# Performance work log

Measured on AMD Instinct MI355X. Metric: run time of the kernel, lower is better.

Reference implementation:

```python
import jax, jax.numpy as jnp
import numpy as np

DIM = 768
HEADS = 12
HEAD_DIM = DIM // HEADS


def setup_inputs() -> dict:
    key = jax.random.key(0)
    ks = jax.random.split(key, 5)
    B, N = 2, 2048
    x = jax.random.normal(ks[0], (B, N, DIM), dtype=jnp.float32)
    s = 1.0 / np.sqrt(DIM)
    qkv_w = jax.random.normal(ks[1], (3 * DIM, DIM), dtype=jnp.float32) * s
    qkv_b = jnp.zeros((3 * DIM,), dtype=jnp.float32)
    proj_w = jax.random.normal(ks[2], (DIM, DIM), dtype=jnp.float32) * s
    proj_b = jnp.zeros((DIM,), dtype=jnp.float32)
    return {"x": x, "qkv_w": qkv_w, "qkv_b": qkv_b, "proj_w": proj_w, "proj_b": proj_b}


def reference(x, qkv_w, qkv_b, proj_w, proj_b):
    B, N, C = x.shape
    scale = HEAD_DIM ** -0.5
    qkv = x @ qkv_w.T + qkv_b                      # [B,N,3C]
    qkv = qkv.reshape(B, N, 3, HEADS, HEAD_DIM)
    q = qkv[:, :, 0].transpose(0, 2, 1, 3)         # [B,H,N,D]
    k = qkv[:, :, 1].transpose(0, 2, 1, 3)
    v = qkv[:, :, 2].transpose(0, 2, 1, 3)
    attn = jnp.einsum('bhnd,bhmd->bhnm', q, k) * scale
    attn = jax.nn.softmax(attn, axis=-1)
    out = jnp.einsum('bhnm,bhmd->bhnd', attn, v)   # [B,H,N,D]
    out = out.transpose(0, 2, 1, 3).reshape(B, N, C)
    return out @ proj_w.T + proj_b
```

## Files before the change

kernel.cpp:

```cpp
#include <hip/hip_runtime.h>
#include <hip/hip_bf16.h>

typedef __bf16 bf16x8 __attribute__((ext_vector_type(8)));
typedef float f32x4 __attribute__((ext_vector_type(4)));
typedef float f32x16 __attribute__((ext_vector_type(16)));

#define SEQ   2048
#define NHEAD 12
#define NBH   24
#define QSCALE 0.18033688011112042f

#define CP16(g, l) __builtin_amdgcn_global_load_lds( \
    (const __attribute__((address_space(1))) unsigned int*)(g), \
    (__attribute__((address_space(3))) unsigned int*)(l), 16, 0, 0)

__device__ __forceinline__ unsigned short f2bf(float f) {
  unsigned int u = __builtin_bit_cast(unsigned int, f);
  u += 0x7FFFu + ((u >> 16) & 1u);
  return (unsigned short)(u >> 16);
}
__device__ __forceinline__ unsigned int packbf2_trunc(float lo, float hi) {
  return __builtin_amdgcn_perm(__builtin_bit_cast(unsigned int, hi),
                               __builtin_bit_cast(unsigned int, lo), 0x07060302u);
}

#define NX4  786432
#define NW14 442368
__global__ __launch_bounds__(256) void cvt3_kernel(const float4* __restrict__ x,
                                                   const float4* __restrict__ w1,
                                                   const float4* __restrict__ w2,
                                                   ushort4* __restrict__ xo,
                                                   ushort4* __restrict__ w1o,
                                                   ushort4* __restrict__ w2o) {
  int i = blockIdx.x * 256 + threadIdx.x;
  const float4* s;
  ushort4* d;
  int j = i;
  if (i < NX4)               { s = x;  d = xo; }
  else if (i < NX4 + NW14)   { s = w1; d = w1o; j = i - NX4; }
  else                       { s = w2; d = w2o; j = i - (NX4 + NW14); }
  float4 v = s[j];
  ushort4 r;
  r.x = f2bf(v.x); r.y = f2bf(v.y); r.z = f2bf(v.z); r.w = f2bf(v.w);
  d[j] = r;
}

template <int BM, int BN, int MODE>
__global__ __launch_bounds__(256) void gemm_kernel(const unsigned short* __restrict__ X,
                                                   const unsigned short* __restrict__ W,
                                                   const float* __restrict__ bias,
                                                   unsigned short* __restrict__ Qb,
                                                   unsigned short* __restrict__ Kb,
                                                   unsigned short* __restrict__ Vtb,
                                                   float* __restrict__ Out) {
  constexpr int K = 768, BK = 64, NKT = K / BK;
  constexpr int WM = BM / 2, WN = BN / 2;
  constexpr int MT = WM / 16, NT = WN / 16;
  __shared__ __align__(16) unsigned short Xs[2][BM * BK];
  __shared__ __align__(16) unsigned short Ws[2][BN * BK];

  const int tid = threadIdx.x;
  const int w = tid >> 6, lane = tid & 63, quad = lane >> 4, m16 = lane & 15;
  const int wm = w & 1, wn = w >> 1;
  const int row0 = blockIdx.y * BM, col0 = blockIdx.x * BN;

  f32x4 acc[MT][NT];
#pragma unroll
  for (int mt = 0; mt < MT; ++mt)
#pragma unroll
    for (int nt = 0; nt < NT; ++nt) acc[mt][nt] = (f32x4){0.f, 0.f, 0.f, 0.f};

#pragma unroll
  for (int j = 0; j < BM / 32; ++j) {
    int e = tid + 256 * j, r = e >> 3, c8 = e & 7;
    CP16(X + (size_t)(row0 + r) * 768 + ((c8 ^ (r & 7)) << 3), &Xs[0][e * 8]);
  }
#pragma unroll
  for (int j = 0; j < BN / 32; ++j) {
    int e = tid + 256 * j, r = e >> 3, c8 = e & 7;
    CP16(W + (size_t)(col0 + r) * 768 + ((c8 ^ (r & 7)) << 3), &Ws[0][e * 8]);
  }

#pragma unroll 2
  for (int kt = 0; kt < NKT; ++kt) {
    const int cur = kt & 1;
    __syncthreads();

    bf16x8 a[2][MT], b[2][NT];
#pragma unroll
    for (int ks = 0; ks < 2; ++ks) {
      const int sw = ((quad + 4 * ks) ^ (m16 & 7)) << 3;
#pragma unroll
      for (int mt = 0; mt < MT; ++mt)
        a[ks][mt] = *(const bf16x8*)(&Xs[cur][(wm * WM + mt * 16 + m16) * BK + sw]);
#pragma unroll
      for (int nt = 0; nt < NT; ++nt)
        b[ks][nt] = *(const bf16x8*)(&Ws[cur][(wn * WN + nt * 16 + m16) * BK + sw]);
    }

    if (kt < NKT - 1) {
      const int k0n = (kt + 1) * BK, nb = 1 - cur;
#pragma unroll
      for (int j = 0; j < BM / 32; ++j) {
        int e = tid + 256 * j, r = e >> 3, c8 = e & 7;
        CP16(X + (size_t)(row0 + r) * 768 + k0n + ((c8 ^ (r & 7)) << 3), &Xs[nb][e * 8]);
      }
#pragma unroll
      for (int j = 0; j < BN / 32; ++j) {
        int e = tid + 256 * j, r = e >> 3, c8 = e & 7;
        CP16(W + (size_t)(col0 + r) * 768 + k0n + ((c8 ^ (r & 7)) << 3), &Ws[nb][e * 8]);
      }
    }

#pragma unroll
    for (int ks = 0; ks < 2; ++ks)
#pragma unroll
      for (int mt = 0; mt < MT; ++mt)
#pragma unroll
        for (int nt = 0; nt < NT; ++nt)
          acc[mt][nt] = __builtin_amdgcn_mfma_f32_16x16x32_bf16(a[ks][mt], b[ks][nt], acc[mt][nt], 0, 0, 0);
  }

#pragma unroll
  for (int mt = 0; mt < MT; ++mt) {
#pragma unroll
    for (int nt = 0; nt < NT; ++nt) {
      const int m0 = row0 + wm * WM + mt * 16 + quad * 4;
      const int c = col0 + wn * WN + nt * 16 + m16;
      const float bia = bias[c];
      f32x4 v = acc[mt][nt];
      if constexpr (MODE == 0) {
        const int bidx = m0 >> 11, ns = m0 & 2047;
        if (c < 1536) {
          unsigned short* dst;
          float sc;
          int cc;
          if (c < 768) { cc = c; dst = Qb; sc = QSCALE; }
          else         { cc = c - 768; dst = Kb; sc = 1.0f; }
          const int h = cc >> 6, d = cc & 63;
          unsigned short* p = dst + ((size_t)(bidx * NHEAD + h) * SEQ + ns) * 64 + d;
          p[0]   = f2bf((v[0] + bia) * sc);
          p[64]  = f2bf((v[1] + bia) * sc);
          p[128] = f2bf((v[2] + bia) * sc);
          p[192] = f2bf((v[3] + bia) * sc);
        } else {
          const int cc = c - 1536, h = cc >> 6, d = cc & 63;
          const int ns2 = (ns & ~12) | ((ns & 4) << 1) | ((ns & 8) >> 1);
          ushort4 pk;
          pk.x = f2bf(v[0] + bia); pk.y = f2bf(v[1] + bia);
          pk.z = f2bf(v[2] + bia); pk.w = f2bf(v[3] + bia);
          *(ushort4*)(Vtb + ((size_t)(bidx * NHEAD + h) * 64 + d) * SEQ + ns2) = pk;
        }
      } else {
        float* o = Out + (size_t)m0 * 768 + c;
        o[0]       = v[0] + bia;
        o[768]     = v[1] + bia;
        o[2 * 768] = v[2] + bia;
        o[3 * 768] = v[3] + bia;
      }
    }
  }
}

__global__ __launch_bounds__(128) void attn_kernel(const unsigned short* __restrict__ Qb,
                                                   const unsigned short* __restrict__ Kb,
                                                   const unsigned short* __restrict__ Vtb,
                                                   unsigned short* __restrict__ Ab) {
  __shared__ __align__(16) unsigned short Ks[2][64 * 64];
  __shared__ __align__(16) unsigned short Vts[2][64 * 64];

  const int tid = threadIdx.x;
  const int w = tid >> 6, lane = tid & 63, hi = lane >> 5, l32 = lane & 31;
  const int bh = blockIdx.x % NBH, qt = blockIdx.x / NBH;
  const int bb = bh / NHEAD, h = bh % NHEAD;
  const int q0 = qt * 64 + w * 32;

  const unsigned short* Qp = Qb + (size_t)bh * SEQ * 64;
  const unsigned short* Kp = Kb + (size_t)bh * SEQ * 64;
  const unsigned short* Vp = Vtb + (size_t)bh * 64 * SEQ;

  bf16x8 qf[4];
#pragma unroll
  for (int dc = 0; dc < 4; ++dc)
    qf[dc] = *(const bf16x8*)(Qp + (size_t)(q0 + l32) * 64 + dc * 16 + hi * 8);

#pragma unroll
  for (int j = 0; j < 4; ++j) {
    int e = tid + 128 * j, r = e >> 3, c8 = e & 7;
    CP16(Kp + (size_t)r * 64 + ((c8 ^ (r & 7)) << 3), &Ks[0][e * 8]);
    CP16(Vp + (size_t)r * SEQ + ((c8 ^ (r & 7)) << 3), &Vts[0][e * 8]);
  }

  f32x16 o[2] = {};
  float m_i = -3.0e38f, l_i = 0.f;

  for (int kt = 0; kt < 32; ++kt) {
    const int cur = kt & 1;
    __syncthreads();

    const unsigned short* Kc = Ks[cur];
    const unsigned short* Vc = Vts[cur];
    bf16x8 kf[2][4], vf[2][4];
#pragma unroll
    for (int t32 = 0; t32 < 2; ++t32)
#pragma unroll
      for (int dc = 0; dc < 4; ++dc)
        kf[t32][dc] = *(const bf16x8*)(Kc + (t32 * 32 + l32) * 64 + ((((dc << 1) | hi) ^ (l32 & 7)) << 3));
#pragma unroll
    for (int dt = 0; dt < 2; ++dt)
#pragma unroll
      for (int cc = 0; cc < 4; ++cc)
        vf[dt][cc] = *(const bf16x8*)(Vc + (dt * 32 + l32) * 64 + ((((cc << 1) | hi) ^ (l32 & 7)) << 3));

    if (kt < 31) {
      const int kn = kt + 1, nb = 1 - cur;
#pragma unroll
      for (int j = 0; j < 4; ++j) {
        int e = tid + 128 * j, r = e >> 3, c8 = e & 7;
        CP16(Kp + (size_t)(kn * 64 + r) * 64 + ((c8 ^ (r & 7)) << 3), &Ks[nb][e * 8]);
        CP16(Vp + (size_t)r * SEQ + kn * 64 + ((c8 ^ (r & 7)) << 3), &Vts[nb][e * 8]);
      }
    }

    f32x16 st[2];
#pragma unroll
    for (int t32 = 0; t32 < 2; ++t32) {
      f32x16 s = {};
#pragma unroll
      for (int dc = 0; dc < 4; ++dc)
        s = __builtin_amdgcn_mfma_f32_32x32x16_bf16(kf[t32][dc], qf[dc], s, 0, 0, 0);
      st[t32] = s;
    }

    float tmax = st[0][0];
#pragma unroll
    for (int t32 = 0; t32 < 2; ++t32)
#pragma unroll
      for (int e = 0; e < 16; ++e) tmax = fmaxf(tmax, st[t32][e]);
    tmax = fmaxf(tmax, __shfl_xor(tmax, 32));
    const float mnew = fmaxf(m_i, tmax);
    const float alpha = __builtin_amdgcn_exp2f(m_i - mnew);
    float ssum = 0.f;
    unsigned int pf[2][8];
#pragma unroll
    for (int t32 = 0; t32 < 2; ++t32) {
      float pv[16];
#pragma unroll
      for (int e = 0; e < 16; ++e) { pv[e] = __builtin_amdgcn_exp2f(st[t32][e] - mnew); ssum += pv[e]; }
#pragma unroll
      for (int e2 = 0; e2 < 8; ++e2)
        pf[t32][e2] = packbf2_trunc(pv[2 * e2], pv[2 * e2 + 1]);
    }
    ssum += __shfl_xor(ssum, 32);
    l_i = l_i * alpha + ssum;
    m_i = mnew;
    o[0] *= alpha;
    o[1] *= alpha;

#pragma unroll
    for (int t32 = 0; t32 < 2; ++t32) {
#pragma unroll
      for (int hh = 0; hh < 2; ++hh) {
        bf16x8 pfrag = __builtin_bit_cast(bf16x8,
            make_uint4(pf[t32][hh * 4], pf[t32][hh * 4 + 1], pf[t32][hh * 4 + 2], pf[t32][hh * 4 + 3]));
        const int cc = 2 * t32 + hh;
#pragma unroll
        for (int dt = 0; dt < 2; ++dt)
          o[dt] = __builtin_amdgcn_mfma_f32_32x32x16_bf16(vf[dt][cc], pfrag, o[dt], 0, 0, 0);
      }
    }
  }

  const float rl = __builtin_amdgcn_rcpf(l_i);
  unsigned short* base = Ab + ((size_t)bb * SEQ + q0 + l32) * 768 + h * 64;
#pragma unroll
  for (int dt = 0; dt < 2; ++dt) {
#pragma unroll
    for (int run = 0; run < 4; ++run) {
      ushort4 pk;
      pk.x = f2bf(o[dt][run * 4 + 0] * rl);
      pk.y = f2bf(o[dt][run * 4 + 1] * rl);
      pk.z = f2bf(o[dt][run * 4 + 2] * rl);
      pk.w = f2bf(o[dt][run * 4 + 3] * rl);
      *(ushort4*)(base + dt * 32 + run * 8 + hi * 4) = pk;
    }
  }
}

extern "C" void kernel_launch(void* const* d_in, const int* in_sizes, int n_in,
                              void* d_out, int out_size, void* d_ws, size_t ws_size,
                              hipStream_t stream) {
  const float* x      = (const float*)d_in[0];
  const float* qkv_w  = (const float*)d_in[1];
  const float* qkv_b  = (const float*)d_in[2];
  const float* proj_w = (const float*)d_in[3];
  const float* proj_b = (const float*)d_in[4];
  float* out = (float*)d_out;

  unsigned short* xb  = (unsigned short*)d_ws;
  unsigned short* wqb = xb + 3145728;
  unsigned short* wpb = wqb + 1769472;
  unsigned short* Qb  = wpb + 589824;
  unsigned short* Kb  = Qb + 3145728;
  unsigned short* Vtb = Kb + 3145728;
  unsigned short* Ab  = Vtb + 3145728;

  cvt3_kernel<<<5376, 256, 0, stream>>>((const float4*)x, (const float4*)qkv_w, (const float4*)proj_w,
                                        (ushort4*)xb, (ushort4*)wqb, (ushort4*)wpb);
  gemm_kernel<128, 96, 0><<<dim3(24, 32), 256, 0, stream>>>(xb, wqb, qkv_b, Qb, Kb, Vtb, nullptr);
  attn_kernel<<<768, 128, 0, stream>>>(Qb, Kb, Vtb, Ab);
  gemm_kernel<64, 96, 1><<<dim3(8, 64), 256, 0, stream>>>(Ab, wpb, proj_b, nullptr, nullptr, nullptr, out);
}
```

Measured before the change: 168.9 us.

## Split attention over two KV halves and merge partials in a combine kernel

```diff
diff --git a/kernel.cpp b/kernel.cpp
--- a/kernel.cpp
+++ b/kernel.cpp
@@ -18,6 +18,9 @@
   unsigned int u = __builtin_bit_cast(unsigned int, f);
   u += 0x7FFFu + ((u >> 16) & 1u);
   return (unsigned short)(u >> 16);
+}
+__device__ __forceinline__ float bfu2f(unsigned int lo16_as_hi) {
+  return __builtin_bit_cast(float, lo16_as_hi);
 }
 __device__ __forceinline__ unsigned int packbf2_trunc(float lo, float hi) {
   return __builtin_amdgcn_perm(__builtin_bit_cast(unsigned int, hi),
@@ -165,19 +168,23 @@
 __global__ __launch_bounds__(128) void attn_kernel(const unsigned short* __restrict__ Qb,
                                                    const unsigned short* __restrict__ Kb,
                                                    const unsigned short* __restrict__ Vtb,
-                                                   unsigned short* __restrict__ Ab) {
+                                                   unsigned short* __restrict__ O0,
+                                                   unsigned short* __restrict__ O1,
+                                                   float2* __restrict__ ml) {
   __shared__ __align__(16) unsigned short Ks[2][64 * 64];
   __shared__ __align__(16) unsigned short Vts[2][64 * 64];
 
   const int tid = threadIdx.x;
   const int w = tid >> 6, lane = tid & 63, hi = lane >> 5, l32 = lane & 31;
-  const int bh = blockIdx.x % NBH, qt = blockIdx.x / NBH;
+  const int bh = blockIdx.x % NBH;
+  const int rest = blockIdx.x / NBH;
+  const int qt = rest & 31, half = rest >> 5;
   const int bb = bh / NHEAD, h = bh % NHEAD;
   const int q0 = qt * 64 + w * 32;
 
   const unsigned short* Qp = Qb + (size_t)bh * SEQ * 64;
-  const unsigned short* Kp = Kb + (size_t)bh * SEQ * 64;
-  const unsigned short* Vp = Vtb + (size_t)bh * 64 * SEQ;
+  const unsigned short* Kp = Kb + (size_t)bh * SEQ * 64 + (size_t)half * 16 * 4096;
+  const unsigned short* Vp = Vtb + (size_t)bh * 64 * SEQ + half * 1024;
 
   bf16x8 qf[4];
 #pragma unroll
@@ -194,7 +201,7 @@
   f32x16 o[2] = {};
   float m_i = -3.0e38f, l_i = 0.f;
 
-  for (int kt = 0; kt < 32; ++kt) {
+  for (int kt = 0; kt < 16; ++kt) {
     const int cur = kt & 1;
     __syncthreads();
 
@@ -212,7 +219,7 @@
       for (int cc = 0; cc < 4; ++cc)
         vf[dt][cc] = *(const bf16x8*)(Vc + (dt * 32 + l32) * 64 + ((((cc << 1) | hi) ^ (l32 & 7)) << 3));
 
-    if (kt < 31) {
+    if (kt < 15) {
       const int kn = kt + 1, nb = 1 - cur;
 #pragma unroll
       for (int j = 0; j < 4; ++j) {
@@ -271,20 +278,55 @@
     }
   }
 
-  const float rl = __builtin_amdgcn_rcpf(l_i);
-  unsigned short* base = Ab + ((size_t)bb * SEQ + q0 + l32) * 768 + h * 64;
+  unsigned short* base = (half ? O1 : O0) + ((size_t)bb * SEQ + q0 + l32) * 768 + h * 64;
 #pragma unroll
   for (int dt = 0; dt < 2; ++dt) {
 #pragma unroll
     for (int run = 0; run < 4; ++run) {
       ushort4 pk;
-      pk.x = f2bf(o[dt][run * 4 + 0] * rl);
-      pk.y = f2bf(o[dt][run * 4 + 1] * rl);
-      pk.z = f2bf(o[dt][run * 4 + 2] * rl);
-      pk.w = f2bf(o[dt][run * 4 + 3] * rl);
+      pk.x = f2bf(o[dt][run * 4 + 0]);
+      pk.y = f2bf(o[dt][run * 4 + 1]);
+      pk.z = f2bf(o[dt][run * 4 + 2]);
+      pk.w = f2bf(o[dt][run * 4 + 3]);
       *(ushort4*)(base + dt * 32 + run * 8 + hi * 4) = pk;
     }
   }
+  if (hi == 0)
+    ml[(size_t)half * (NBH * SEQ) + bh * SEQ + q0 + l32] = make_float2(m_i, l_i);
+}
+
+__global__ __launch_bounds__(256) void combine_kernel(unsigned short* __restrict__ O0,
+                                                      const unsigned short* __restrict__ O1,
+                                                      const float2* __restrict__ ml) {
+  const int gid = blockIdx.x * 256 + threadIdx.x;
+  const int t = gid / 48, ci = gid - t * 48;
+  const int ch0 = ci * 16, h = ch0 >> 6;
+  const int mlrow = ((t >> 11) * NHEAD + h) * SEQ + (t & 2047);
+  const float2 ml0 = ml[mlrow], ml1 = ml[NBH * SEQ + mlrow];
+  const float m = fmaxf(ml0.x, ml1.x);
+  const float a0 = __builtin_amdgcn_exp2f(ml0.x - m);
+  const float a1 = __builtin_amdgcn_exp2f(ml1.x - m);
+  const float rl = __builtin_amdgcn_rcpf(a0 * ml0.y + a1 * ml1.y);
+  const float s0 = a0 * rl, s1 = a1 * rl;
+  unsigned short* p0 = O0 + (size_t)t * 768 + ch0;
+  const unsigned short* p1 = O1 + (size_t)t * 768 + ch0;
+  uint4 x[2], y[2];
+  x[0] = *(const uint4*)p0;       x[1] = *(const uint4*)(p0 + 8);
+  y[0] = *(const uint4*)p1;       y[1] = *(const uint4*)(p1 + 8);
+#pragma unroll
+  for (int q = 0; q < 2; ++q) {
+    unsigned int* xu = (unsigned int*)&x[q];
+    const unsigned int* yu = (const unsigned int*)&y[q];
+#pragma unroll
+    for (int e = 0; e < 4; ++e) {
+      const unsigned int u0 = xu[e], u1 = yu[e];
+      const float lo = bfu2f(u0 << 16) * s0 + bfu2f(u1 << 16) * s1;
+      const float hi = bfu2f(u0 & 0xFFFF0000u) * s0 + bfu2f(u1 & 0xFFFF0000u) * s1;
+      xu[e] = ((unsigned int)f2bf(hi) << 16) | f2bf(lo);
+    }
+  }
+  *(uint4*)p0 = x[0];
+  *(uint4*)(p0 + 8) = x[1];
 }
 
 extern "C" void kernel_launch(void* const* d_in, const int* in_sizes, int n_in,
@@ -308,6 +350,7 @@
   cvt3_kernel<<<5376, 256, 0, stream>>>((const float4*)x, (const float4*)qkv_w, (const float4*)proj_w,
                                         (ushort4*)xb, (ushort4*)wqb, (ushort4*)wpb);
   gemm_kernel<128, 96, 0><<<dim3(24, 32), 256, 0, stream>>>(xb, wqb, qkv_b, Qb, Kb, Vtb, nullptr);
-  attn_kernel<<<768, 128, 0, stream>>>(Qb, Kb, Vtb, Ab);
+  attn_kernel<<<1536, 128, 0, stream>>>(Qb, Kb, Vtb, Ab, xb, (float2*)wqb);
+  combine_kernel<<<768, 256, 0, stream>>>(Ab, xb, (const float2*)wqb);
   gemm_kernel<64, 96, 1><<<dim3(8, 64), 256, 0, stream>>>(Ab, wpb, proj_b, nullptr, nullptr, nullptr, out);
 }
```

New measurement: 173.0 us. +2.4%, slower.

## Fuse fp32-to-bf16 conversion into GEMM tile staging, drop convert kernel

Applied to the files above, without the earlier changes.

```diff
diff --git a/kernel.cpp b/kernel.cpp
--- a/kernel.cpp
+++ b/kernel.cpp
@@ -23,31 +23,27 @@
   return __builtin_amdgcn_perm(__builtin_bit_cast(unsigned int, hi),
                                __builtin_bit_cast(unsigned int, lo), 0x07060302u);
 }
-
-#define NX4  786432
-#define NW14 442368
-__global__ __launch_bounds__(256) void cvt3_kernel(const float4* __restrict__ x,
-                                                   const float4* __restrict__ w1,
-                                                   const float4* __restrict__ w2,
-                                                   ushort4* __restrict__ xo,
-                                                   ushort4* __restrict__ w1o,
-                                                   ushort4* __restrict__ w2o) {
-  int i = blockIdx.x * 256 + threadIdx.x;
-  const float4* s;
-  ushort4* d;
-  int j = i;
-  if (i < NX4)               { s = x;  d = xo; }
-  else if (i < NX4 + NW14)   { s = w1; d = w1o; j = i - NX4; }
-  else                       { s = w2; d = w2o; j = i - (NX4 + NW14); }
-  float4 v = s[j];
-  ushort4 r;
-  r.x = f2bf(v.x); r.y = f2bf(v.y); r.z = f2bf(v.z); r.w = f2bf(v.w);
-  d[j] = r;
+__device__ __forceinline__ unsigned int packbf2_rne(float lo, float hi) {
+  unsigned int r;
+  asm("v_cvt_pk_bf16_f32 %0, %1, %2" : "=v"(r) : "v"(lo), "v"(hi));
+  return r;
+}
+__device__ __forceinline__ void stage_f32_bf16(const float* __restrict__ src,
+                                               unsigned short* dst) {
+  const float4 a0 = *(const float4*)src;
+  const float4 a1 = *(const float4*)(src + 4);
+  uint4 u;
+  u.x = packbf2_rne(a0.x, a0.y);
+  u.y = packbf2_rne(a0.z, a0.w);
+  u.z = packbf2_rne(a1.x, a1.y);
+  u.w = packbf2_rne(a1.z, a1.w);
+  *(uint4*)dst = u;
 }
 
 template <int BM, int BN, int MODE>
-__global__ __launch_bounds__(256) void gemm_kernel(const unsigned short* __restrict__ X,
-                                                   const unsigned short* __restrict__ W,
+__global__ __launch_bounds__(256) void gemm_kernel(const float* __restrict__ Xf,
+                                                   const unsigned short* __restrict__ Xh,
+                                                   const float* __restrict__ Wf,
                                                    const float* __restrict__ bias,
                                                    unsigned short* __restrict__ Qb,
                                                    unsigned short* __restrict__ Kb,
@@ -70,22 +66,39 @@
 #pragma unroll
     for (int nt = 0; nt < NT; ++nt) acc[mt][nt] = (f32x4){0.f, 0.f, 0.f, 0.f};
 
-#pragma unroll
-  for (int j = 0; j < BM / 32; ++j) {
-    int e = tid + 256 * j, r = e >> 3, c8 = e & 7;
-    CP16(X + (size_t)(row0 + r) * 768 + ((c8 ^ (r & 7)) << 3), &Xs[0][e * 8]);
-  }
-#pragma unroll
-  for (int j = 0; j < BN / 32; ++j) {
-    int e = tid + 256 * j, r = e >> 3, c8 = e & 7;
-    CP16(W + (size_t)(col0 + r) * 768 + ((c8 ^ (r & 7)) << 3), &Ws[0][e * 8]);
-  }
+  auto stageA = [&](int k0, int b) {
+#pragma unroll
+    for (int j = 0; j < BM / 32; ++j) {
+      int e = tid + 256 * j, r = e >> 3, c8 = e & 7;
+      const int off = k0 + ((c8 ^ (r & 7)) << 3);
+      if constexpr (MODE == 0)
+        stage_f32_bf16(Xf + (size_t)(row0 + r) * 768 + off, &Xs[b][e * 8]);
+      else
+        CP16(Xh + (size_t)(row0 + r) * 768 + off, &Xs[b][e * 8]);
+    }
+  };
+  auto stageB = [&](int k0, int b) {
+#pragma unroll
+    for (int j = 0; j < BN / 32; ++j) {
+      int e = tid + 256 * j, r = e >> 3, c8 = e & 7;
+      const int off = k0 + ((c8 ^ (r & 7)) << 3);
+      stage_f32_bf16(Wf + (size_t)(col0 + r) * 768 + off, &Ws[b][e * 8]);
+    }
+  };
+
+  stageA(0, 0);
+  stageB(0, 0);
 
 #pragma unroll 2
   for (int kt = 0; kt < NKT; ++kt) {
     const int cur = kt & 1;
     __syncthreads();
 
+    if (kt < NKT - 1) {
+      stageA((kt + 1) * BK, 1 - cur);
+      stageB((kt + 1) * BK, 1 - cur);
+    }
+
     bf16x8 a[2][MT], b[2][NT];
 #pragma unroll
     for (int ks = 0; ks < 2; ++ks) {
@@ -96,20 +109,6 @@
 #pragma unroll
       for (int nt = 0; nt < NT; ++nt)
         b[ks][nt] = *(const bf16x8*)(&Ws[cur][(wn * WN + nt * 16 + m16) * BK + sw]);
-    }
-
-    if (kt < NKT - 1) {
-      const int k0n = (kt + 1) * BK, nb = 1 - cur;
-#pragma unroll
-      for (int j = 0; j < BM / 32; ++j) {
-        int e = tid + 256 * j, r = e >> 3, c8 = e & 7;
-        CP16(X + (size_t)(row0 + r) * 768 + k0n + ((c8 ^ (r & 7)) << 3), &Xs[nb][e * 8]);
-      }
-#pragma unroll
-      for (int j = 0; j < BN / 32; ++j) {
-        int e = tid + 256 * j, r = e >> 3, c8 = e & 7;
-        CP16(W + (size_t)(col0 + r) * 768 + k0n + ((c8 ^ (r & 7)) << 3), &Ws[nb][e * 8]);
-      }
     }
 
 #pragma unroll
@@ -297,17 +296,14 @@
   const float* proj_b = (const float*)d_in[4];
   float* out = (float*)d_out;
 
-  unsigned short* xb  = (unsigned short*)d_ws;
-  unsigned short* wqb = xb + 3145728;
-  unsigned short* wpb = wqb + 1769472;
-  unsigned short* Qb  = wpb + 589824;
+  unsigned short* Qb  = (unsigned short*)d_ws;
   unsigned short* Kb  = Qb + 3145728;
   unsigned short* Vtb = Kb + 3145728;
   unsigned short* Ab  = Vtb + 3145728;
 
-  cvt3_kernel<<<5376, 256, 0, stream>>>((const float4*)x, (const float4*)qkv_w, (const float4*)proj_w,
-                                        (ushort4*)xb, (ushort4*)wqb, (ushort4*)wpb);
-  gemm_kernel<128, 96, 0><<<dim3(24, 32), 256, 0, stream>>>(xb, wqb, qkv_b, Qb, Kb, Vtb, nullptr);
+  gemm_kernel<128, 96, 0><<<dim3(24, 32), 256, 0, stream>>>(x, nullptr, qkv_w, qkv_b,
+                                                            Qb, Kb, Vtb, nullptr);
   attn_kernel<<<768, 128, 0, stream>>>(Qb, Kb, Vtb, Ab);
-  gemm_kernel<64, 96, 1><<<dim3(8, 64), 256, 0, stream>>>(Ab, wpb, proj_b, nullptr, nullptr, nullptr, out);
-}
+  gemm_kernel<64, 96, 1><<<dim3(8, 64), 256, 0, stream>>>(nullptr, Ab, proj_w, proj_b,
+                                                          nullptr, nullptr, nullptr, out);
+}
```

Result: slower. 185.5 us (+9.8%).
